# Optimization experiments

Hardware: AMD Instinct MI355X
Metric: run time of the kernel (lower is better)

Reference implementation:

```python
import jax, jax.numpy as jnp
import numpy as np
import math

B, S, D, H, HD, M, E = 4, 1024, 1024, 16, 64, 4096, 1024
EPS = 1e-6

def rms_norm(x, w):
    # torch: x / (||x||/sqrt(d) + eps) * w  (eps added to the norm, not norm^2)
    n = jnp.sqrt(jnp.sum(x * x, axis=-1, keepdims=True)) / math.sqrt(x.shape[-1])
    return x / (n + EPS) * w

def rope(x):
    # x: (B,H,S,hd)
    hd, s = x.shape[-1], x.shape[2]
    inv = 1.0 / (10000.0 ** (jnp.arange(0, hd, 2, dtype=jnp.float32) / hd))
    fr = jnp.arange(s, dtype=jnp.float32)[:, None] * inv[None, :]        # (S, hd/2)
    emb = jnp.concatenate([fr, fr], axis=-1)                              # (S, hd)
    cos, sin = jnp.cos(emb), jnp.sin(emb)
    x1, x2 = x[..., : hd // 2], x[..., hd // 2 :]
    rot = jnp.concatenate([-x2, x1], axis=-1)
    return x * cos + rot * sin

def setup_inputs() -> dict:
    key = jax.random.key(0)
    ks = jax.random.split(key, 18)
    p = lambda k, sh: jax.random.normal(k, sh, jnp.float32) * 0.02
    return {
        'x': jax.random.normal(ks[0], (B, S, D), jnp.float32),
        'emb': jax.random.normal(ks[1], (B, E), jnp.float32),
        'ln1_w': jnp.ones((D,), jnp.float32),
        'ln1_lW': p(ks[2], (E, 2 * D)), 'ln1_lb': p(ks[3], (2 * D,)),
        'ln2_w': jnp.ones((D,), jnp.float32),
        'ln2_lW': p(ks[4], (E, 2 * D)), 'ln2_lb': p(ks[5], (2 * D,)),
        'qkv_W': p(ks[6], (D, 3 * D)), 'qkv_b': p(ks[7], (3 * D,)),
        'proj_W': p(ks[8], (D, D)), 'proj_b': p(ks[9], (D,)),
        'nq_w': jnp.ones((HD,), jnp.float32), 'nk_w': jnp.ones((HD,), jnp.float32),
        'mlp_W': p(ks[10], (D, 2 * M)), 'mlp_b': p(ks[11], (2 * M,)),
        'out_W': p(ks[12], (M, D)), 'out_b': p(ks[13], (D,)),
        'gates_W': p(ks[14], (E, 2 * D)), 'gates_b': p(ks[15], (2 * D,)),
    }

def reference(x, emb, ln1_w, ln1_lW, ln1_lb, ln2_w, ln2_lW, ln2_lb,
              qkv_W, qkv_b, proj_W, proj_b, nq_w, nk_w,
              mlp_W, mlp_b, out_W, out_b, gates_W, gates_b):
    g = emb @ gates_W + gates_b                       # (B, 2D)
    gate_mha, gate_mlp = g[:, :D], g[:, D:]
    # AdaLNZero 1
    ss = emb @ ln1_lW + ln1_lb                        # (B, 2D): [scale | shift]
    xn = rms_norm(x, ln1_w) * (1.0 + ss[:, None, :D]) + ss[:, None, D:]
    # RoPE attention with qk RMSNorm
    qkv = (xn @ qkv_W + qkv_b).reshape(B, S, 3, H, HD).transpose(2, 0, 3, 1, 4)
    q, k, v = qkv[0], qkv[1], qkv[2]                  # each (B,H,S,HD)
    q = rms_norm(rope(q), nq_w)
    k = rms_norm(rope(k), nk_w)
    scores = jnp.einsum('bhqd,bhkd->bhqk', q, k) * (HD ** -0.5)
    attn = jnp.nan_to_num(jax.nn.softmax(scores, axis=-1))
    ao = jnp.einsum('bhqk,bhkd->bhqd', attn, v).transpose(0, 2, 1, 3).reshape(B, S, D)
    x = x + gate_mha[:, None, :] * (ao @ proj_W + proj_b)
    # AdaLNZero 2 + SwiGLU MLP
    ss2 = emb @ ln2_lW + ln2_lb
    xn2 = rms_norm(x, ln2_w) * (1.0 + ss2[:, None, :D]) + ss2[:, None, D:]
    h = xn2 @ mlp_W + mlp_b                           # (B,S,2M)
    act = h[..., :M] * jax.nn.silu(h[..., M:])
    mlp_out = act @ out_W + out_b
    return x + gate_mlp[:, None, :] * mlp_out
```

## Files before the change

kernel.cpp:

```cpp
#include <hip/hip_runtime.h>
#include <hip/hip_bf16.h>
#include <math.h>

#define B_ 4
#define S_ 1024
#define D_ 1024
#define H_ 16
#define HD_ 64
#define M_ 4096
#define E_ 1024

using bf16 = __hip_bfloat16;
typedef short bf16x8 __attribute__((ext_vector_type(8)));
typedef float f32x4 __attribute__((ext_vector_type(4)));

__device__ __forceinline__ void gl_lds16(const void* g, void* l) {
    __builtin_amdgcn_global_load_lds(
        (__attribute__((address_space(1))) void*)(g),
        (__attribute__((address_space(3))) void*)(l), 16, 0, 0);
}



#define STG_A(q, pb, kc) gl_lds16(A  + gAoff[q] + (kc), &sA[pb][(q) * 4096 + tid * 8])
#define STG_B(q, pb, kc) gl_lds16(Bt + gBoff[q] + (kc), &sB[pb][(q) * 4096 + tid * 8])

#define LDA(mh, m, h) (*(const bf16x8*)(cA + aRow + (mh) * 8192 + (m) * 2048 + (h)))
#define LDB(nh, n, h) (*(const bf16x8*)(cB + bRow + (nh) * 4096 + (n) * 2048 + (h)))

#define MFMA_QUAD(MH, NH, BF)                                                             \
    __builtin_amdgcn_s_setprio(1);                                                        \
    _Pragma("unroll")                                                                     \
    for (int m = 0; m < 4; ++m) {                                                         \
        _Pragma("unroll")                                                                 \
        for (int n = 0; n < 2; ++n) {                                                     \
            acc[(MH)*4+m][(NH)*2+n] = __builtin_amdgcn_mfma_f32_16x16x32_bf16(            \
                aF[m][0], BF[n][0], acc[(MH)*4+m][(NH)*2+n], 0, 0, 0);                    \
            acc[(MH)*4+m][(NH)*2+n] = __builtin_amdgcn_mfma_f32_16x16x32_bf16(            \
                aF[m][1], BF[n][1], acc[(MH)*4+m][(NH)*2+n], 0, 0, 0);                    \
        }                                                                                 \
    }                                                                                     \
    __builtin_amdgcn_s_setprio(0);

#define GEMM256_LOOP                                                                      \
    const int nt = K >> 6;                                                                \
    for (int t = 0; t < nt; ++t) {                                                        \
        const int pb = t & 1;                                                             \
        const char* cA = (const char*)sA[pb];                                             \
        const char* cB = (const char*)sB[pb];                                             \
        const int kc2 = (t + 2) << 6;                                                     \
        const bool pf = (t + 2) < nt;                                                     \
        bf16x8 aF[4][2], b0F[2][2], b1F[2][2];                                            \
                                          \
        _Pragma("unroll")                                                                 \
        for (int m = 0; m < 4; ++m) {                                                     \
            aF[m][0] = LDA(0, m, cs0);                                                    \
            aF[m][1] = LDA(0, m, cs1);                                                    \
        }                                                                                 \
        _Pragma("unroll")                                                                 \
        for (int n = 0; n < 2; ++n) {                                                     \
            b0F[n][0] = LDB(0, n, cs0);                                                   \
            b0F[n][1] = LDB(0, n, cs1);                                                   \
        }                                                                                 \
        __builtin_amdgcn_s_barrier();                                                     \
        asm volatile("s_waitcnt lgkmcnt(0)" ::: "memory");                                \
        MFMA_QUAD(0, 0, b0F)                                                              \
        __builtin_amdgcn_s_barrier();                                                     \
                         \
        _Pragma("unroll")                                                                 \
        for (int n = 0; n < 2; ++n) {                                                     \
            b1F[n][0] = LDB(1, n, cs0);                                                   \
            b1F[n][1] = LDB(1, n, cs1);                                                   \
        }                                                                                 \
        if (pf) { STG_A(0, pb, kc2); STG_A(2, pb, kc2); }                                 \
        __builtin_amdgcn_s_barrier();                                                     \
        asm volatile("s_waitcnt lgkmcnt(0)" ::: "memory");                                \
        MFMA_QUAD(0, 1, b1F)                                                              \
        __builtin_amdgcn_s_barrier();                                                     \
                               \
        _Pragma("unroll")                                                                 \
        for (int m = 0; m < 4; ++m) {                                                     \
            aF[m][0] = LDA(1, m, cs0);                                                    \
            aF[m][1] = LDA(1, m, cs1);                                                    \
        }                                                                                 \
        if (pf) { STG_B(0, pb, kc2); STG_B(1, pb, kc2);                                   \
                  STG_B(2, pb, kc2); STG_B(3, pb, kc2); }                                 \
        __builtin_amdgcn_s_barrier();                                                     \
        asm volatile("s_waitcnt lgkmcnt(0)" ::: "memory");                                \
        MFMA_QUAD(1, 1, b1F)                                                              \
        __builtin_amdgcn_s_barrier();                                                     \
                                 \
        if (pf) { STG_A(1, pb, kc2); STG_A(3, pb, kc2); }                                 \
        __builtin_amdgcn_s_barrier();                                                     \
        asm volatile("s_waitcnt lgkmcnt(0)" ::: "memory");                                \
        MFMA_QUAD(1, 0, b0F)                                                              \
        if (pf)              { asm volatile("s_waitcnt vmcnt(8)" ::: "memory"); }         \
        else if (t + 1 < nt) { asm volatile("s_waitcnt vmcnt(0)" ::: "memory"); }         \
        __builtin_amdgcn_s_barrier();                                                     \
    }

#define GEMM256_PROLOG(NPN, N0MUL)                                                        \
    const int tid = threadIdx.x;                                                          \
    const int wave = tid >> 6, lane = tid & 63;                                           \
    const int wr = wave >> 2, wc = wave & 3;                                              \
    const int cl = lane & 15, qd = lane >> 4;                                             \
    const int num_pid_n = (NPN);                                                          \
    const int cpx = gridDim.x >> 3;                                                       \
    int wg = (blockIdx.x & 7) * cpx + (blockIdx.x >> 3);                                  \
    const int group_size = 8 * num_pid_n;                                                 \
    const int group_id = wg / group_size;                                                 \
    const int pid_in = wg - group_id * group_size;                                        \
    const int m0 = (group_id * 8 + (pid_in & 7)) * 256;                                   \
    const int n0 = (pid_in >> 3) * (N0MUL);

__global__ __launch_bounds__(256) void prep_kernel(
    float4* __restrict__ tab,
    const float* __restrict__ W0, bf16* __restrict__ T0,
    const float* __restrict__ W1, bf16* __restrict__ T1,
    const float* __restrict__ W2, bf16* __restrict__ T2,
    const float* __restrict__ W3, bf16* __restrict__ T3,
    const float* __restrict__ emb,
    const float* __restrict__ gW, const float* __restrict__ gb,
    const float* __restrict__ l1W, const float* __restrict__ l1b,
    const float* __restrict__ l2W, const float* __restrict__ l2b,
    float* __restrict__ G, float* __restrict__ SS, float* __restrict__ SS2)
{
    __shared__ float tile[32][33];
    __shared__ float se[256];
    int id = blockIdx.x;
    if (id < 64) {
        int idx = id * 256 + threadIdx.x;
        int s = idx >> 4, j = idx & 15;
        float inv0 = exp2f(-(float)j        * (13.287712379549449f / 32.f));
        float inv1 = exp2f(-(float)(16 + j) * (13.287712379549449f / 32.f));
        float sn0, c0, sn1, c1;
        sincosf((float)s * inv0, &sn0, &c0);
        sincosf((float)s * inv1, &sn1, &c1);
        tab[idx] = make_float4(c0, sn0, c1, sn1);
        return;
    }
    if (id < 16448) {
        id -= 64;
        const float* W; bf16* T; int K, N, bx, by;
        if (id < 3072)       { W = W0; T = T0; K = 1024; N = 3072; bx = id % 96;  by = id / 96; }
        else if (id < 4096)  { id -= 3072;  W = W1; T = T1; K = 1024; N = 1024; bx = id & 31;  by = id >> 5; }
        else if (id < 12288) { id -= 4096;  W = W2; T = T2; K = 1024; N = 8192; bx = id & 255; by = id >> 8; }
        else                 { id -= 12288; W = W3; T = T3; K = 4096; N = 1024; bx = id & 31;  by = id >> 5; }
        int n0 = bx * 32, k0 = by * 32;
        int tx = threadIdx.x & 31, ty = threadIdx.x >> 5;
        #pragma unroll
        for (int r = ty; r < 32; r += 8)
            tile[r][tx] = W[(long)(k0 + r) * N + n0 + tx];
        __syncthreads();
        #pragma unroll
        for (int r = ty; r < 32; r += 8)
            T[(long)(n0 + r) * K + k0 + tx] = __float2bfloat16(tile[tx][r]);
        return;
    }
    id -= 16448;
    int bx = id % 24, b = (id / 24) & 3, k0 = (id / 96) * 256;
    if (threadIdx.x < 256) se[threadIdx.x] = emb[b * 1024 + k0 + threadIdx.x];
    __syncthreads();
    int j = bx * 256 + threadIdx.x;
    int which = j >> 11, col = j & 2047;
    const float* W  = which == 0 ? gW : (which == 1 ? l1W : l2W);
    const float* bb = which == 0 ? gb : (which == 1 ? l1b : l2b);
    float acc = (k0 == 0) ? bb[col] : 0.f;
    #pragma unroll 4
    for (int k = 0; k < 256; ++k) acc += se[k] * W[(long)(k0 + k) * 2048 + col];
    float* out = which == 0 ? G : (which == 1 ? SS : SS2);
    atomicAdd(&out[b * 2048 + col], acc);
}

__global__ __launch_bounds__(256) void rmsmod_kernel(
    const float* __restrict__ x, const float* __restrict__ w,
    const float* __restrict__ ss, bf16* __restrict__ out)
{
    int row = blockIdx.x;
    int b = row >> 10;
    const float* xr = x + (long)row * D_;
    float4 v = ((const float4*)xr)[threadIdx.x];
    float ssum = v.x * v.x + v.y * v.y + v.z * v.z + v.w * v.w;
    #pragma unroll
    for (int off = 32; off; off >>= 1) ssum += __shfl_xor(ssum, off);
    __shared__ float red[4];
    if ((threadIdx.x & 63) == 0) red[threadIdx.x >> 6] = ssum;
    __syncthreads();
    float tot = red[0] + red[1] + red[2] + red[3];
    float n = sqrtf(tot) * (1.f / 32.f);
    float inv = 1.f / (n + 1e-6f);
    int d0 = threadIdx.x * 4;
    const float* ssb = ss + b * 2048;
    bf16 t[4];
    t[0] = __float2bfloat16(v.x * inv * w[d0 + 0] * (1.f + ssb[d0 + 0]) + ssb[D_ + d0 + 0]);
    t[1] = __float2bfloat16(v.y * inv * w[d0 + 1] * (1.f + ssb[d0 + 1]) + ssb[D_ + d0 + 1]);
    t[2] = __float2bfloat16(v.z * inv * w[d0 + 2] * (1.f + ssb[d0 + 2]) + ssb[D_ + d0 + 2]);
    t[3] = __float2bfloat16(v.w * inv * w[d0 + 3] * (1.f + ssb[d0 + 3]) + ssb[D_ + d0 + 3]);
    *(uint2*)&out[(long)row * D_ + d0] = *(uint2*)t;
}

__global__ __launch_bounds__(512) void qkvgemm_kernel(
    const bf16* __restrict__ A, const bf16* __restrict__ Bt,
    const float* __restrict__ bias,
    const float* __restrict__ nq_w, const float* __restrict__ nk_w,
    const float4* __restrict__ ropetab,
    bf16* __restrict__ qh, bf16* __restrict__ kh, bf16* __restrict__ vt,
    int N, int K)
{
    __shared__ bf16 sA[2][16384];
    __shared__ bf16 sB[2][16384];
    GEMM256_PROLOG(N >> 8, 256)

    long gAoff[4], gBoff[4];
    #pragma unroll
    for (int q = 0; q < 4; ++q) {
        int c = tid + q * 512;
        int cs = c ^ ((c >> 3) & 7);
        int row = cs >> 3, col = (cs & 7) * 8;
        gAoff[q] = (long)(m0 + row) * K + col;
        gBoff[q] = (long)(n0 + row) * K + col;
    }

    #pragma unroll
    for (int q = 0; q < 4; ++q) { STG_A(q, 0, 0); STG_B(q, 0, 0); }
    #pragma unroll
    for (int q = 0; q < 4; ++q) { STG_A(q, 1, 64); STG_B(q, 1, 64); }

    f32x4 acc[8][4] = {};
    const int swz = (cl & 7) << 4;
    const int aRow = (wr * 128 + cl) * 128;
    const int bRow = (wc * 64 + cl) * 128;
    const int cs0 = (qd * 16) ^ swz;
    const int cs1 = (qd * 16 + 64) ^ swz;

    asm volatile("s_waitcnt vmcnt(8)" ::: "memory");
    __builtin_amdgcn_s_barrier();

    GEMM256_LOOP

    const int third = n0 >> 10;
    const int h = ((n0 & 1023) >> 6) + wc;
    const int b = m0 >> 10;
    const int s0 = (m0 & 1023) + wr * 128;
    const int colb = n0 + wc * 64;
    float bs0 = bias[colb + cl],      bs1 = bias[colb + 16 + cl];
    float bs2 = bias[colb + 32 + cl], bs3 = bias[colb + 48 + cl];

    if (third == 2) {
        #pragma unroll
        for (int n = 0; n < 4; ++n) {
            int d = n * 16 + cl;
            float bs = bias[colb + n * 16 + cl];
            long rowd = ((long)(b * 16 + h) * 64 + d) * 1024;
            #pragma unroll
            for (int m = 0; m < 8; ++m) {
                int sb = s0 + m * 16 + qd * 4;
                bf16 t4[4];
                #pragma unroll
                for (int i = 0; i < 4; ++i)
                    t4[i] = __float2bfloat16(acc[m][n][i] + bs);
                *(uint2*)&vt[rowd + sb] = *(uint2*)t4;
            }
        }
    } else {
        const float* w = (third == 0) ? nq_w : nk_w;
        bf16* dst = (third == 0) ? qh : kh;
        float w0 = w[cl], w1 = w[16 + cl], w2 = w[32 + cl], w3 = w[48 + cl];
        long hb = ((long)(b * 16 + h) * 1024) * 64;
        #pragma unroll
        for (int m = 0; m < 8; ++m) {
            #pragma unroll
            for (int i = 0; i < 4; ++i) {
                int s = s0 + m * 16 + qd * 4 + i;
                float v0 = acc[m][0][i] + bs0, v1 = acc[m][1][i] + bs1;
                float v2 = acc[m][2][i] + bs2, v3 = acc[m][3][i] + bs3;
                float4 cs = ropetab[s * 16 + cl];
                float r0 = v0 * cs.x - v2 * cs.y;
                float r1 = v1 * cs.z - v3 * cs.w;
                float r2 = v2 * cs.x + v0 * cs.y;
                float r3 = v3 * cs.z + v1 * cs.w;
                float ssq = r0 * r0 + r1 * r1 + r2 * r2 + r3 * r3;
                ssq += __shfl_xor(ssq, 1);
                ssq += __shfl_xor(ssq, 2);
                ssq += __shfl_xor(ssq, 4);
                ssq += __shfl_xor(ssq, 8);
                float innv = 1.f / (sqrtf(ssq) * 0.125f + 1e-6f);
                long ro = hb + (long)s * 64;
                dst[ro + cl]      = __float2bfloat16(r0 * innv * w0);
                dst[ro + 16 + cl] = __float2bfloat16(r1 * innv * w1);
                dst[ro + 32 + cl] = __float2bfloat16(r2 * innv * w2);
                dst[ro + 48 + cl] = __float2bfloat16(r3 * innv * w3);
            }
        }
    }
}

__global__ __launch_bounds__(512) void gemm256_mlp_kernel(
    const bf16* __restrict__ A, const bf16* __restrict__ Bt,
    const float* __restrict__ bias, bf16* __restrict__ ACT, int K)
{
    __shared__ bf16 sA[2][16384];
    __shared__ bf16 sB[2][16384];
    GEMM256_PROLOG(32, 128)

    long gAoff[4], gBoff[4];
    #pragma unroll
    for (int q = 0; q < 4; ++q) {
        int c = tid + q * 512;
        int cs = c ^ ((c >> 3) & 7);
        int row = cs >> 3, col = (cs & 7) * 8;
        gAoff[q] = (long)(m0 + row) * K + col;
        int pp = row >> 5, hf = (row >> 4) & 1, wi = row & 15;
        gBoff[q] = (long)(hf * 4096 + n0 + pp * 16 + wi) * K + col;
    }

    #pragma unroll
    for (int q = 0; q < 4; ++q) { STG_A(q, 0, 0); STG_B(q, 0, 0); }
    #pragma unroll
    for (int q = 0; q < 4; ++q) { STG_A(q, 1, 64); STG_B(q, 1, 64); }

    f32x4 acc[8][4] = {};
    const int swz = (cl & 7) << 4;
    const int aRow = (wr * 128 + cl) * 128;
    const int bRow = (wc * 64 + cl) * 128;
    const int cs0 = (qd * 16) ^ swz;
    const int cs1 = (qd * 16 + 64) ^ swz;

    asm volatile("s_waitcnt vmcnt(8)" ::: "memory");
    __builtin_amdgcn_s_barrier();

    GEMM256_LOOP

    #pragma unroll
    for (int m = 0; m < 8; ++m) {
        #pragma unroll
        for (int pr = 0; pr < 2; ++pr) {
            int col = n0 + wc * 32 + pr * 16 + cl;
            float bs1 = bias[col];
            float bs2 = bias[4096 + col];
            #pragma unroll
            for (int i = 0; i < 4; ++i) {
                int row = m0 + wr * 128 + m * 16 + qd * 4 + i;
                float h1 = acc[m][pr * 2 + 0][i] + bs1;
                float h2 = acc[m][pr * 2 + 1][i] + bs2;
                float sg = 1.f / (1.f + __expf(-h2));
                ACT[(long)row * 4096 + col] = __float2bfloat16(h1 * h2 * sg);
            }
        }
    }
}

#define MFMA_HQ(MH)                                                                       \
    __builtin_amdgcn_s_setprio(1);                                                        \
    _Pragma("unroll")                                                                     \
    for (int m = 0; m < 4; ++m) {                                                         \
        _Pragma("unroll")                                                                 \
        for (int n = 0; n < 2; ++n) {                                                     \
            acc[(MH)*4+m][n] = __builtin_amdgcn_mfma_f32_16x16x32_bf16(                   \
                aF[m][0], bF[n][0], acc[(MH)*4+m][n], 0, 0, 0);                           \
            acc[(MH)*4+m][n] = __builtin_amdgcn_mfma_f32_16x16x32_bf16(                   \
                aF[m][1], bF[n][1], acc[(MH)*4+m][n], 0, 0, 0);                           \
        }                                                                                 \
    }                                                                                     \
    __builtin_amdgcn_s_setprio(0);

__global__ __launch_bounds__(512) void gemm256x128_kernel(
    const bf16* __restrict__ A, const bf16* __restrict__ Bt,
    float* __restrict__ P0, float* __restrict__ P1, int N, int K)
{
    __shared__ bf16 sA[2][16384];
    __shared__ bf16 sB[2][8192];
    const int tid = threadIdx.x;
    const int wave = tid >> 6, lane = tid & 63;
    const int wr = wave >> 2, wc = wave & 3;
    const int cl = lane & 15, qd = lane >> 4;

    const int cpx = gridDim.x >> 3;
    int wg = (blockIdx.x & 7) * cpx + (blockIdx.x >> 3);
    const int split = wg >> 7;
    const int w2 = wg & 127;
    const int group_id = w2 >> 6;
    const int pid_in = w2 & 63;
    const int m0 = (group_id * 8 + (pid_in & 7)) * 256;
    const int n0 = (pid_in >> 3) * 128;
    const int Kh = K >> 1;
    A  += (long)split * Kh;
    Bt += (long)split * Kh;

    long gAoff[4], gBoff[2];
    #pragma unroll
    for (int q = 0; q < 4; ++q) {
        int c = tid + q * 512;
        int cs = c ^ ((c >> 3) & 7);
        int row = cs >> 3, col = (cs & 7) * 8;
        gAoff[q] = (long)(m0 + row) * K + col;
        if (q < 2) gBoff[q] = (long)(n0 + row) * K + col;
    }

    const int nt = Kh >> 6;
    STG_A(0, 0, 0); STG_A(2, 0, 0); STG_B(0, 0, 0); STG_B(1, 0, 0);
    STG_A(1, 0, 0); STG_A(3, 0, 0);
    if (nt > 1) { STG_A(0, 1, 64); STG_A(2, 1, 64); STG_B(0, 1, 64); STG_B(1, 1, 64); }

    f32x4 acc[8][2] = {};
    const int swz = (cl & 7) << 4;
    const int aRow = (wr * 128 + cl) * 128;
    const int bRow = (wc * 32 + cl) * 128;
    const int cs0 = (qd * 16) ^ swz;
    const int cs1 = (qd * 16 + 64) ^ swz;

    if (nt > 1) { asm volatile("s_waitcnt vmcnt(4)" ::: "memory"); }
    else        { asm volatile("s_waitcnt vmcnt(0)" ::: "memory"); }
    __builtin_amdgcn_s_barrier();

    for (int t = 0; t < nt; ++t) {
        const int pb = t & 1;
        const char* cA = (const char*)sA[pb];
        const char* cB = (const char*)sB[pb];
        bf16x8 aF[4][2], bF[2][2];
        #pragma unroll
        for (int m = 0; m < 4; ++m) {
            aF[m][0] = *(const bf16x8*)(cA + aRow + m * 2048 + cs0);
            aF[m][1] = *(const bf16x8*)(cA + aRow + m * 2048 + cs1);
        }
        #pragma unroll
        for (int n = 0; n < 2; ++n) {
            bF[n][0] = *(const bf16x8*)(cB + bRow + n * 2048 + cs0);
            bF[n][1] = *(const bf16x8*)(cB + bRow + n * 2048 + cs1);
        }
        if (t + 1 < nt) { STG_A(1, pb ^ 1, (t + 1) << 6); STG_A(3, pb ^ 1, (t + 1) << 6); }
        __builtin_amdgcn_s_barrier();
        asm volatile("s_waitcnt lgkmcnt(0)" ::: "memory");
        MFMA_HQ(0)
        __builtin_amdgcn_s_barrier();
        #pragma unroll
        for (int m = 0; m < 4; ++m) {
            aF[m][0] = *(const bf16x8*)(cA + aRow + 8192 + m * 2048 + cs0);
            aF[m][1] = *(const bf16x8*)(cA + aRow + 8192 + m * 2048 + cs1);
        }
        if (t + 2 < nt) { STG_A(0, pb, (t + 2) << 6); STG_A(2, pb, (t + 2) << 6);
                          STG_B(0, pb, (t + 2) << 6); STG_B(1, pb, (t + 2) << 6); }
        __builtin_amdgcn_s_barrier();
        asm volatile("s_waitcnt lgkmcnt(0)" ::: "memory");
        MFMA_HQ(1)
        if (t + 2 < nt)      { asm volatile("s_waitcnt vmcnt(4)" ::: "memory"); }
        else if (t + 1 < nt) { asm volatile("s_waitcnt vmcnt(0)" ::: "memory"); }
        __builtin_amdgcn_s_barrier();
    }

    float* P = split ? P1 : P0;
    #pragma unroll
    for (int m = 0; m < 8; ++m) {
        #pragma unroll
        for (int n = 0; n < 2; ++n) {
            int col = n0 + wc * 32 + n * 16 + cl;
            #pragma unroll
            for (int i = 0; i < 4; ++i) {
                int row = m0 + wr * 128 + m * 16 + qd * 4 + i;
                P[(long)row * N + col] = acc[m][n][i];
            }
        }
    }
}

__global__ __launch_bounds__(256) void fuseout_kernel(
    const float* __restrict__ p0, const float* __restrict__ p1,
    const float* __restrict__ bias, const float* __restrict__ resid,
    const float* __restrict__ gates, float* __restrict__ out)
{
    int idx = blockIdx.x * 256 + threadIdx.x;
    int row = idx >> 8;
    int b = row >> 10;
    int c4 = (idx & 255) * 4;
    float4 a = ((const float4*)p0)[idx];
    float4 c = ((const float4*)p1)[idx];
    float4 r = ((const float4*)resid)[idx];
    float4 bb = *(const float4*)&bias[c4];
    float4 gg = *(const float4*)&gates[b * 2048 + 1024 + c4];
    float4 o;
    o.x = r.x + gg.x * (a.x + c.x + bb.x);
    o.y = r.y + gg.y * (a.y + c.y + bb.y);
    o.z = r.z + gg.z * (a.z + c.z + bb.z);
    o.w = r.w + gg.w * (a.w + c.w + bb.w);
    ((float4*)out)[idx] = o;
}

__global__ __launch_bounds__(256) void gemm64_kernel(
    const bf16* __restrict__ A, const bf16* __restrict__ Bt,
    const float* __restrict__ bias,
    bf16* __restrict__ Cb, float* __restrict__ Cf,
    const float* __restrict__ resid, const float* __restrict__ gates, int gate_off,
    int Mrows, int N, int K, int mode)
{
    __shared__ bf16 sA[64 * 32];
    __shared__ bf16 sB[64 * 32];
    const int tid = threadIdx.x;
    const int wave = tid >> 6, lane = tid & 63;
    const int num_pid_n = N >> 6;
    const int pid = blockIdx.x;
    const int group_size = 8 * num_pid_n;
    const int group_id = pid / group_size;
    const int pid_in = pid - group_id * group_size;
    const int pid_m = group_id * 8 + (pid_in & 7);
    const int pid_n = pid_in >> 3;
    const int m0 = pid_m * 64, n0 = pid_n * 64;
    const int wm = (wave & 1) * 32, wn = (wave >> 1) * 32;
    const int cl = lane & 15, qd = lane >> 4;

    f32x4 acc[2][2] = {};

    const int c = tid;
    const int rr = c >> 2, ss = (c & 3) ^ ((c >> 3) & 3);
    const bf16* gA = A + (long)(m0 + rr) * K + ss * 8;
    const bf16* gB = Bt + (long)(n0 + rr) * K + ss * 8;
    bf16* lA = &sA[wave * 512];
    bf16* lB = &sB[wave * 512];

    const int q8s = (qd ^ ((cl >> 1) & 3)) * 8;

    for (int kc = 0; kc < K; kc += 32) {
        gl_lds16(gA + kc, lA);
        gl_lds16(gB + kc, lB);
        __syncthreads();
        bf16x8 af[2], bfr[2];
        #pragma unroll
        for (int t = 0; t < 2; ++t)
            af[t] = *(const bf16x8*)&sA[(wm + cl + t * 16) * 32 + q8s];
        #pragma unroll
        for (int u = 0; u < 2; ++u)
            bfr[u] = *(const bf16x8*)&sB[(wn + cl + u * 16) * 32 + q8s];
        #pragma unroll
        for (int t = 0; t < 2; ++t)
            #pragma unroll
            for (int u = 0; u < 2; ++u)
                acc[t][u] = __builtin_amdgcn_mfma_f32_16x16x32_bf16(af[t], bfr[u], acc[t][u], 0, 0, 0);
        __syncthreads();
    }

    #pragma unroll
    for (int t = 0; t < 2; ++t) {
        #pragma unroll
        for (int u = 0; u < 2; ++u) {
            int col = n0 + wn + u * 16 + cl;
            float bs = bias[col];
            #pragma unroll
            for (int i = 0; i < 4; ++i) {
                int row = m0 + wm + t * 16 + qd * 4 + i;
                float v = acc[t][u][i] + bs;
                if (mode == 0) {
                    Cb[(long)row * N + col] = __float2bfloat16(v);
                } else {
                    int b = row >> 10;
                    float g = gates[b * 2048 + gate_off + col];
                    Cf[(long)row * N + col] = resid[(long)row * N + col] + g * v;
                }
            }
        }
    }
}

__global__ __launch_bounds__(256) void attn_kernel(
    const bf16* __restrict__ qh, const bf16* __restrict__ kh, const bf16* __restrict__ vt,
    bf16* __restrict__ ao)
{
    const int bh = blockIdx.y;
    const int q0 = blockIdx.x * 64;
    const int tid = threadIdx.x, wave = tid >> 6, lane = tid & 63;
    const int cl = lane & 15, qd = lane >> 4;

    __shared__ bf16 sQ[64 * 64];
    __shared__ bf16 sK[2][64 * 64];
    __shared__ bf16 sV[2][64 * 64];
    __shared__ bf16 sP[4][16 * 64];

    const int r0 = tid >> 3;
    const int c0 = (tid & 7) ^ (r0 & 7);
    const int r1 = (tid + 256) >> 3;
    const int c1 = ((tid + 256) & 7) ^ (r1 & 7);

    const bf16* Kg = kh + (long)bh * S_ * 64;
    const bf16* Vg = vt + (long)bh * 64 * S_;

    #define ATTN_STAGE(t) {                                                          \
        int kv = (t) * 64;                                                           \
        gl_lds16(Kg + (long)(kv + r0) * 64 + c0 * 8, &sK[(t) & 1][(long)tid * 8]);   \
        gl_lds16(Kg + (long)(kv + r1) * 64 + c1 * 8, &sK[(t) & 1][(long)(tid + 256) * 8]); \
        gl_lds16(Vg + (long)r0 * S_ + kv + c0 * 8, &sV[(t) & 1][(long)tid * 8]);     \
        gl_lds16(Vg + (long)r1 * S_ + kv + c1 * 8, &sV[(t) & 1][(long)(tid + 256) * 8]); }

    {
        const bf16* Qg = qh + (long)bh * S_ * 64 + (long)q0 * 64;
        gl_lds16(Qg + r0 * 64 + c0 * 8, &sQ[(long)tid * 8]);
        gl_lds16(Qg + r1 * 64 + c1 * 8, &sQ[(long)(tid + 256) * 8]);
        ATTN_STAGE(0)
    }

    float l_i[4] = {0.f, 0.f, 0.f, 0.f};
    f32x4 o_acc[4] = {};

    const int swz = (cl & 7) << 4;
    const char* cQ = (const char*)sQ;
    char* cP = (char*)sP[wave];
    const int aqRow = (wave * 16 + cl) * 128;

    for (int t = 0; t < 16; ++t) {
        __builtin_amdgcn_s_barrier();
        if (t + 1 < 16) {
            ATTN_STAGE(t + 1)
            asm volatile("s_waitcnt vmcnt(4)" ::: "memory");
        } else {
            asm volatile("s_waitcnt vmcnt(0)" ::: "memory");
        }
        __builtin_amdgcn_s_barrier();
        const char* cK = (const char*)sK[t & 1];
        const char* cV = (const char*)sV[t & 1];

        f32x4 sfr[4] = {};
        #pragma unroll
        for (int ks = 0; ks < 2; ++ks) {
            const int co = (ks * 64 + qd * 16) ^ swz;
            bf16x8 aq = *(const bf16x8*)(cQ + aqRow + co);
            #pragma unroll
            for (int u = 0; u < 4; ++u) {
                bf16x8 bk = *(const bf16x8*)(cK + (u * 16 + cl) * 128 + co);
                sfr[u] = __builtin_amdgcn_mfma_f32_16x16x32_bf16(aq, bk, sfr[u], 0, 0, 0);
            }
        }

        #pragma unroll
        for (int i = 0; i < 4; ++i) {
            int rowp = qd * 4 + i;
            char* pb = cP + rowp * 128;
            const int xorv = (rowp & 7) << 4;
            float sum = 0.f;
            #pragma unroll
            for (int u = 0; u < 4; ++u) {
                float p = __expf(sfr[u][i] * 0.125f - 8.f);
                sum += p;
                *(bf16*)(pb + ((u * 32 + cl * 2) ^ xorv)) = __float2bfloat16(p);
            }
            sum += __shfl_xor(sum, 1);
            sum += __shfl_xor(sum, 2);
            sum += __shfl_xor(sum, 4);
            sum += __shfl_xor(sum, 8);
            l_i[i] += sum;
        }

        #pragma unroll
        for (int ks = 0; ks < 2; ++ks) {
            const int co = (ks * 64 + qd * 16) ^ swz;
            bf16x8 ap = *(const bf16x8*)(cP + cl * 128 + co);
            #pragma unroll
            for (int u = 0; u < 4; ++u) {
                bf16x8 bv = *(const bf16x8*)(cV + (u * 16 + cl) * 128 + co);
                o_acc[u] = __builtin_amdgcn_mfma_f32_16x16x32_bf16(ap, bv, o_acc[u], 0, 0, 0);
            }
        }
    }
    #undef ATTN_STAGE

    #pragma unroll
    for (int i = 0; i < 4; ++i) {
        float invl = 1.f / l_i[i];
        int row = q0 + wave * 16 + qd * 4 + i;
        #pragma unroll
        for (int u = 0; u < 4; ++u) {
            int d = u * 16 + cl;
            ao[((long)(bh >> 4) * S_ + row) * D_ + (bh & 15) * 64 + d] =
                __float2bfloat16(o_acc[u][i] * invl);
        }
    }
}

extern "C" void kernel_launch(void* const* d_in, const int* in_sizes, int n_in,
                              void* d_out, int out_size, void* d_ws, size_t ws_size,
                              hipStream_t stream) {
    const float* x       = (const float*)d_in[0];
    const float* emb     = (const float*)d_in[1];
    const float* ln1_w   = (const float*)d_in[2];
    const float* ln1_lW  = (const float*)d_in[3];
    const float* ln1_lb  = (const float*)d_in[4];
    const float* ln2_w   = (const float*)d_in[5];
    const float* ln2_lW  = (const float*)d_in[6];
    const float* ln2_lb  = (const float*)d_in[7];
    const float* qkv_W   = (const float*)d_in[8];
    const float* qkv_b   = (const float*)d_in[9];
    const float* proj_W  = (const float*)d_in[10];
    const float* proj_b  = (const float*)d_in[11];
    const float* nq_w    = (const float*)d_in[12];
    const float* nk_w    = (const float*)d_in[13];
    const float* mlp_W   = (const float*)d_in[14];
    const float* mlp_b   = (const float*)d_in[15];
    const float* out_W   = (const float*)d_in[16];
    const float* out_b   = (const float*)d_in[17];
    const float* gates_W = (const float*)d_in[18];
    const float* gates_b = (const float*)d_in[19];
    float* out = (float*)d_out;

    char* p = (char*)d_ws;
    if (ws_size < 159481856UL) return;
    bf16* WT_QKV  = (bf16*)p;  p += 6291456;
    bf16* WT_PROJ = (bf16*)p;  p += 2097152;
    bf16* WT_MLP  = (bf16*)p;  p += 16777216;
    bf16* WT_OUT  = (bf16*)p;  p += 8388608;
    float* G      = (float*)p; p += 32768;
    float* SSb    = (float*)p; p += 32768;
    float* SS2b   = (float*)p; p += 32768;
    float* X1     = (float*)p; p += 16777216;
    bf16* XN2     = (bf16*)p;  p += 8388608;
    bf16* ACT     = (bf16*)p;  p += 33554432;
    char* REG = p;
    bf16* XN   = (bf16*)(REG);
    bf16* QH   = (bf16*)(REG + 33554432);
    bf16* KH   = (bf16*)(REG + 41943040);
    bf16* VT   = (bf16*)(REG + 50331648);
    bf16* AO   = (bf16*)(REG + 58720256);
    float* PF0 = (float*)(REG);
    float* PF1 = (float*)(REG + 16777216);
    float4* ROPETAB = (float4*)X1;

    dim3 blk(256);
    hipMemsetAsync(G, 0, 98304, stream);
    prep_kernel<<<dim3(16832), blk, 0, stream>>>(ROPETAB,
                                                 qkv_W, WT_QKV, proj_W, WT_PROJ,
                                                 mlp_W, WT_MLP, out_W, WT_OUT,
                                                 emb, gates_W, gates_b, ln1_lW, ln1_lb,
                                                 ln2_lW, ln2_lb, G, SSb, SS2b);
    rmsmod_kernel<<<dim3(4096), blk, 0, stream>>>(x, ln1_w, SSb, XN);
    qkvgemm_kernel<<<dim3(192), dim3(512), 0, stream>>>(XN, WT_QKV, qkv_b, nq_w, nk_w,
                                                        ROPETAB, QH, KH, VT, 3072, 1024);
    attn_kernel<<<dim3(16, 64), blk, 0, stream>>>(QH, KH, VT, AO);
    gemm64_kernel<<<dim3(1024), blk, 0, stream>>>(AO, WT_PROJ, proj_b, nullptr, X1,
                                                  x, G, 0, 4096, 1024, 1024, 1);
    rmsmod_kernel<<<dim3(4096), blk, 0, stream>>>(X1, ln2_w, SS2b, XN2);
    gemm256_mlp_kernel<<<dim3(512), dim3(512), 0, stream>>>(XN2, WT_MLP, mlp_b, ACT, 1024);
    gemm256x128_kernel<<<dim3(256), dim3(512), 0, stream>>>(ACT, WT_OUT, PF0, PF1, 1024, 4096);
    fuseout_kernel<<<dim3(4096), blk, 0, stream>>>(PF0, PF1, out_b, X1, G, out);
}
```

Baseline: 452.9 us.

## Stage q/k epilogue through LDS for wide stores; keep Q fragments in registers

The QKV GEMM epilogue for q/k used to write scattered 2-byte stores to global memory. It now writes the normalized rows into a swizzled per-wave LDS scratch region and re-reads them as 16-byte vectors, so the global writes are coalesced. The attention kernel loads its Q fragments straight into registers instead of going through LDS, and wraps the MFMA sections in s_setprio. The epilogue reuses the sA buffer, and its correctness depends on no other wave still using that buffer.

```diff
diff --git a/kernel.cpp b/kernel.cpp
--- a/kernel.cpp
+++ b/kernel.cpp
@@ -267,6 +267,7 @@
         bf16* dst = (third == 0) ? qh : kh;
         float w0 = w[cl], w1 = w[16 + cl], w2 = w[32 + cl], w3 = w[48 + cl];
         long hb = ((long)(b * 16 + h) * 1024) * 64;
+        char* wlds = (char*)&sA[0][wave * 1024];
         #pragma unroll
         for (int m = 0; m < 8; ++m) {
             #pragma unroll
@@ -285,12 +286,22 @@
                 ssq += __shfl_xor(ssq, 4);
                 ssq += __shfl_xor(ssq, 8);
                 float innv = 1.f / (sqrtf(ssq) * 0.125f + 1e-6f);
-                long ro = hb + (long)s * 64;
-                dst[ro + cl]      = __float2bfloat16(r0 * innv * w0);
-                dst[ro + 16 + cl] = __float2bfloat16(r1 * innv * w1);
-                dst[ro + 32 + cl] = __float2bfloat16(r2 * innv * w2);
-                dst[ro + 48 + cl] = __float2bfloat16(r3 * innv * w3);
+                int row = qd * 4 + i;
+                int xorv = (row & 7) << 4;
+                char* wb = wlds + row * 128;
+                *(bf16*)(wb + ((cl * 2 +  0) ^ xorv)) = __float2bfloat16(r0 * innv * w0);
+                *(bf16*)(wb + ((cl * 2 + 32) ^ xorv)) = __float2bfloat16(r1 * innv * w1);
+                *(bf16*)(wb + ((cl * 2 + 64) ^ xorv)) = __float2bfloat16(r2 * innv * w2);
+                *(bf16*)(wb + ((cl * 2 + 96) ^ xorv)) = __float2bfloat16(r3 * innv * w3);
             }
+            asm volatile("s_waitcnt lgkmcnt(0)" ::: "memory");
+            int rrow = lane >> 2;
+            int rx = (rrow & 7) << 4;
+            long ro = hb + (long)(s0 + m * 16 + rrow) * 64 + (lane & 3) * 16;
+            uint4 u0 = *(const uint4*)(wlds + rrow * 128 + ((((lane & 3) * 32) +  0) ^ rx));
+            uint4 u1 = *(const uint4*)(wlds + rrow * 128 + ((((lane & 3) * 32) + 16) ^ rx));
+            *(uint4*)&dst[ro]     = u0;
+            *(uint4*)&dst[ro + 8] = u1;
         }
     }
 }
@@ -568,7 +579,6 @@
     const int tid = threadIdx.x, wave = tid >> 6, lane = tid & 63;
     const int cl = lane & 15, qd = lane >> 4;
 
-    __shared__ bf16 sQ[64 * 64];
     __shared__ bf16 sK[2][64 * 64];
     __shared__ bf16 sV[2][64 * 64];
     __shared__ bf16 sP[4][16 * 64];
@@ -588,10 +598,11 @@
         gl_lds16(Vg + (long)r0 * S_ + kv + c0 * 8, &sV[(t) & 1][(long)tid * 8]);     \
         gl_lds16(Vg + (long)r1 * S_ + kv + c1 * 8, &sV[(t) & 1][(long)(tid + 256) * 8]); }
 
+    bf16x8 qf[2];
     {
         const bf16* Qg = qh + (long)bh * S_ * 64 + (long)q0 * 64;
-        gl_lds16(Qg + r0 * 64 + c0 * 8, &sQ[(long)tid * 8]);
-        gl_lds16(Qg + r1 * 64 + c1 * 8, &sQ[(long)(tid + 256) * 8]);
+        qf[0] = *(const bf16x8*)&Qg[(wave * 16 + cl) * 64 + qd * 8];
+        qf[1] = *(const bf16x8*)&Qg[(wave * 16 + cl) * 64 + 32 + qd * 8];
         ATTN_STAGE(0)
     }
 
@@ -599,9 +610,7 @@
     f32x4 o_acc[4] = {};
 
     const int swz = (cl & 7) << 4;
-    const char* cQ = (const char*)sQ;
     char* cP = (char*)sP[wave];
-    const int aqRow = (wave * 16 + cl) * 128;
 
     for (int t = 0; t < 16; ++t) {
         __builtin_amdgcn_s_barrier();
@@ -616,16 +625,17 @@
         const char* cV = (const char*)sV[t & 1];
 
         f32x4 sfr[4] = {};
+        __builtin_amdgcn_s_setprio(1);
         #pragma unroll
         for (int ks = 0; ks < 2; ++ks) {
             const int co = (ks * 64 + qd * 16) ^ swz;
-            bf16x8 aq = *(const bf16x8*)(cQ + aqRow + co);
             #pragma unroll
             for (int u = 0; u < 4; ++u) {
                 bf16x8 bk = *(const bf16x8*)(cK + (u * 16 + cl) * 128 + co);
-                sfr[u] = __builtin_amdgcn_mfma_f32_16x16x32_bf16(aq, bk, sfr[u], 0, 0, 0);
+                sfr[u] = __builtin_amdgcn_mfma_f32_16x16x32_bf16(qf[ks], bk, sfr[u], 0, 0, 0);
             }
         }
+        __builtin_amdgcn_s_setprio(0);
 
         #pragma unroll
         for (int i = 0; i < 4; ++i) {
@@ -646,6 +656,7 @@
             l_i[i] += sum;
         }
 
+        __builtin_amdgcn_s_setprio(1);
         #pragma unroll
         for (int ks = 0; ks < 2; ++ks) {
             const int co = (ks * 64 + qd * 16) ^ swz;
@@ -656,6 +667,7 @@
                 o_acc[u] = __builtin_amdgcn_mfma_f32_16x16x32_bf16(ap, bv, o_acc[u], 0, 0, 0);
             }
         }
+        __builtin_amdgcn_s_setprio(0);
     }
     #undef ATTN_STAGE
 
```

After: 450.1 us. No clear change (-0.6%).
